# Kernel optimization log

Measured on AMD Instinct MI355X. Metric: run time of the kernel, lower is better.

The kernel has to match this reference:

```python
import jax, jax.numpy as jnp
import numpy as np
from jax import lax

B, T, F_IN = 8, 512, 229
C1 = 48            # model_size_conv // 16
C3 = 96            # model_size_conv // 8
D_CONV = 768       # model_size_conv
D_LSTM = 768       # model_size_lstm
N_PITCH = 88       # MAX_MIDI - MIN_MIDI + 1
N_STATE = 5
EMB = 2
LSTM_IN = D_CONV + N_PITCH * EMB   # 944
FC_IN = C3 * (F_IN // 4)           # 96 * 57 = 5472
BN_EPS = 1e-5


def setup_inputs() -> dict:
    key = jax.random.key(0)
    ks = iter(jax.random.split(key, 64))
    nrm = lambda shape, s=0.05: jax.random.normal(next(ks), shape, jnp.float32) * s
    uni = lambda shape: jax.random.uniform(next(ks), shape, jnp.float32, 0.5, 1.5)
    inp = {
        'mel': jax.random.normal(next(ks), (B, T, F_IN), jnp.float32),
        'conv1_w': nrm((C1, 1, 3, 3)), 'conv1_b': nrm((C1,)),
        'bn1_g': uni((C1,)), 'bn1_b': nrm((C1,)), 'bn1_m': nrm((C1,), 0.1), 'bn1_v': uni((C1,)),
        'conv2_w': nrm((C1, C1, 3, 3)), 'conv2_b': nrm((C1,)),
        'bn2_g': uni((C1,)), 'bn2_b': nrm((C1,)), 'bn2_m': nrm((C1,), 0.1), 'bn2_v': uni((C1,)),
        'conv3_w': nrm((C3, C1, 3, 3)), 'conv3_b': nrm((C3,)),
        'bn3_g': uni((C3,)), 'bn3_b': nrm((C3,)), 'bn3_m': nrm((C3,), 0.1), 'bn3_v': uni((C3,)),
        'fc_w': nrm((D_CONV, FC_IN)), 'fc_b': nrm((D_CONV,)),
        'wih1': nrm((4 * D_LSTM, LSTM_IN)), 'whh1': nrm((4 * D_LSTM, D_LSTM)),
        'bih1': nrm((4 * D_LSTM,)), 'bhh1': nrm((4 * D_LSTM,)),
        'wih2': nrm((4 * D_LSTM, D_LSTM)), 'whh2': nrm((4 * D_LSTM, D_LSTM)),
        'bih2': nrm((4 * D_LSTM,)), 'bhh2': nrm((4 * D_LSTM,)),
        'post_w': nrm((N_PITCH * N_STATE, D_LSTM)), 'post_b': nrm((N_PITCH * N_STATE,)),
        'emb_w': nrm((N_STATE, EMB), 1.0),
    }
    return inp


def _conv_bn_relu(x, w, b, g, be, m, v):
    # x: NCHW, w: OIHW, padding 'SAME' == padding=1 for 3x3
    y = lax.conv_general_dilated(x, w, (1, 1), 'SAME', dimension_numbers=('NCHW', 'OIHW', 'NCHW'))
    y = y + b[None, :, None, None]
    scale = (g / jnp.sqrt(v + BN_EPS))[None, :, None, None]
    y = (y - m[None, :, None, None]) * scale + be[None, :, None, None]
    return jax.nn.relu(y)


def _maxpool12(x):
    # MaxPool2d((1,2)) on NCHW, floor mode
    return lax.reduce_window(x, -jnp.inf, lax.max, (1, 1, 1, 2), (1, 1, 1, 2), 'VALID')


def _lstm_cell(x, h, c, wih, whh, bih, bhh):
    z = x @ wih.T + h @ whh.T + bih + bhh
    i, f, g, o = jnp.split(z, 4, axis=-1)
    c = jax.nn.sigmoid(f) * c + jax.nn.sigmoid(i) * jnp.tanh(g)
    h = jax.nn.sigmoid(o) * jnp.tanh(c)
    return h, c


def _forward(mel, conv1_w, conv1_b, bn1_g, bn1_b, bn1_m, bn1_v,
             conv2_w, conv2_b, bn2_g, bn2_b, bn2_m, bn2_v,
             conv3_w, conv3_b, bn3_g, bn3_b, bn3_m, bn3_v,
             fc_w, fc_b, wih1, whh1, bih1, bhh1, wih2, whh2, bih2, bhh2,
             post_w, post_b, emb_w):
    b = mel.shape[0]
    # --- ConvStack acoustic model (eval mode: dropout = identity) ---
    x = mel[:, None]                                  # (B,1,T,F)
    x = _conv_bn_relu(x, conv1_w, conv1_b, bn1_g, bn1_b, bn1_m, bn1_v)
    x = _conv_bn_relu(x, conv2_w, conv2_b, bn2_g, bn2_b, bn2_m, bn2_v)
    x = _maxpool12(x)
    x = _conv_bn_relu(x, conv3_w, conv3_b, bn3_g, bn3_b, bn3_m, bn3_v)
    x = _maxpool12(x)                                 # (B,C3,T,F//4)
    x = x.transpose(0, 2, 1, 3).reshape(b, -1, FC_IN) # (B,T,C3*F//4)
    acoustic = x @ fc_w.T + fc_b                      # (B,T,768)

    def step(carry, a_t):
        h1, c1, h2, c2, prev = carry                  # prev: (B,88) int32
        emb = emb_w[prev].reshape(prev.shape[0], N_PITCH * EMB)
        xt = jnp.concatenate([a_t, emb], axis=-1)     # (B,944)
        h1n, c1n = _lstm_cell(xt, h1, c1, wih1, whh1, bih1, bhh1)
        h2n, c2n = _lstm_cell(h1n, h2, c2, wih2, whh2, bih2, bhh2)
        logits = (h2n @ post_w.T + post_b).reshape(-1, N_PITCH, N_STATE)
        nprev = jnp.argmax(logits, axis=-1).astype(jnp.int32)  # argmax(softmax)==argmax(logits)
        return (h1n, c1n, h2n, c2n, nprev), logits

    z = jnp.zeros((b, D_LSTM), mel.dtype)
    prev0 = jnp.zeros((b, N_PITCH), jnp.int32)
    _, logits = lax.scan(step, (z, z, z, z, prev0), acoustic.transpose(1, 0, 2))
    return logits.transpose(1, 0, 2, 3)               # (B,T,88,N_STATE)


def reference(mel, conv1_w, conv1_b, bn1_g, bn1_b, bn1_m, bn1_v,
              conv2_w, conv2_b, bn2_g, bn2_b, bn2_m, bn2_v,
              conv3_w, conv3_b, bn3_g, bn3_b, bn3_m, bn3_v,
              fc_w, fc_b, wih1, whh1, bih1, bhh1, wih2, whh2, bih2, bhh2,
              post_w, post_b, emb_w):
    return _forward(mel, conv1_w, conv1_b, bn1_g, bn1_b, bn1_m, bn1_v,
                    conv2_w, conv2_b, bn2_g, bn2_b, bn2_m, bn2_v,
                    conv3_w, conv3_b, bn3_g, bn3_b, bn3_m, bn3_v,
                    fc_w, fc_b, wih1, whh1, bih1, bhh1, wih2, whh2, bih2, bhh2,
                    post_w, post_b, emb_w)
```

## Files before the change

kernel.cpp:

```cpp
#include <hip/hip_runtime.h>
#include <math.h>

#define WS_C3   0u
#define WS_C2CH 22413312u
#define WS_AC   28104192u
#define WS_A1   0u
#define WS_ST   31249920u

__device__ __forceinline__ float sigm(float x){ return 1.0f / (1.0f + expf(-x)); }

__device__ __forceinline__ void cstore(float* p, float v){
  union { float f; unsigned u; } c; c.f = v;
  __hip_atomic_store((unsigned*)p, c.u, __ATOMIC_RELAXED,
                     __HIP_MEMORY_SCOPE_SYSTEM);
}
__device__ __forceinline__ void cload64(const float* p, float& a, float& b){
  unsigned long long u = __hip_atomic_load((const unsigned long long*)p,
                          __ATOMIC_RELAXED, __HIP_MEMORY_SCOPE_SYSTEM);
  union { unsigned long long u; float f[2]; } c; c.u = u;
  a = c.f[0]; b = c.f[1];
}
__device__ __forceinline__ unsigned cloadu(const unsigned* p){
  return __hip_atomic_load(p, __ATOMIC_RELAXED, __HIP_MEMORY_SCOPE_SYSTEM);
}

#define SLOT 16
#define FLG  4112
__device__ __forceinline__ void gbar(unsigned* sy, unsigned bar, int wg){
  __syncthreads();
  const int tid = threadIdx.x;
  if (tid == 0)
    __hip_atomic_store(&sy[SLOT + wg*16], bar, __ATOMIC_RELAXED,
                       __HIP_MEMORY_SCOPE_SYSTEM);
  if (wg == 255){
    if (tid < 64){
      for (;;){
        unsigned m0 = cloadu(&sy[SLOT + (4*tid + 0)*16]);
        unsigned m1 = cloadu(&sy[SLOT + (4*tid + 1)*16]);
        unsigned m2 = cloadu(&sy[SLOT + (4*tid + 2)*16]);
        unsigned m3 = cloadu(&sy[SLOT + (4*tid + 3)*16]);
        unsigned a = m0 < m1 ? m0 : m1;
        unsigned b = m2 < m3 ? m2 : m3;
        unsigned mn = a < b ? a : b;
        if (__all(mn >= bar)) break;
        __builtin_amdgcn_s_sleep(1);
      }
    }
    __syncthreads();
    __hip_atomic_store(&sy[FLG + tid*16], bar, __ATOMIC_RELAXED,
                       __HIP_MEMORY_SCOPE_SYSTEM);
  } else {
    if (tid == 0){
      while (cloadu(&sy[FLG + wg*16]) < bar)
        __builtin_amdgcn_s_sleep(1);
    }
  }
  __syncthreads();
}

__global__ __launch_bounds__(256) void conv2f_k(
    const float* __restrict__ mel, const float* __restrict__ w1,
    const float* __restrict__ b1, const float* __restrict__ g1,
    const float* __restrict__ be1, const float* __restrict__ m1,
    const float* __restrict__ v1,
    const float* __restrict__ w2, const float* __restrict__ b2,
    const float* __restrict__ g2, const float* __restrict__ be2,
    const float* __restrict__ m2, const float* __restrict__ v2,
    float* __restrict__ c2ch, int t0)
{
  __shared__ float act[3*8*240];
  __shared__ float w2s[48*8*12];
  __shared__ float mel5[5*240];
  __shared__ float w1s[48*12];
  __shared__ float sc1[48], sh1[48], sc2[48], sh2[48];
  int tid = threadIdx.x;
  int b = blockIdx.x / 130, lt = blockIdx.x - b*130;
  int t = t0 - 1 + lt;

  int fg = tid % 29, ocg = tid / 29;
  int f0 = fg * 8, oc0 = ocg * 6;

  if (t < 0 || t > 511){
    if (tid < 232){
      for (int o = 0; o < 6; ++o)
        for (int jj = 0; jj < 4; ++jj){
          int fp = fg*4 + jj;
          if (fp < 114)
            c2ch[((b*48 + oc0 + o)*130 + lt)*114 + fp] = 0.f;
        }
    }
    return;
  }

  for (int idx = tid; idx < 5*240; idx += 256){
    int rr = idx / 240, w = idx - rr*240;
    int tt = t + rr - 2, f = w - 2;
    mel5[idx] = (tt >= 0 && tt < 512 && f >= 0 && f < 229)
                ? mel[(b*512 + tt)*229 + f] : 0.f;
  }
  for (int idx = tid; idx < 48*12; idx += 256){
    int c = idx / 12, q = idx - c*12;
    int kh = q >> 2, kw = q & 3;
    w1s[idx] = (kw < 3) ? w1[c*9 + kh*3 + kw] : 0.f;
  }
  if (tid < 48){
    float s1 = g1[tid] / sqrtf(v1[tid] + 1e-5f);
    sc1[tid] = s1; sh1[tid] = be1[tid] + (b1[tid] - m1[tid]) * s1;
    float s2 = g2[tid] / sqrtf(v2[tid] + 1e-5f);
    sc2[tid] = s2; sh2[tid] = be2[tid] + (b2[tid] - m2[tid]) * s2;
  }

  float acc[6][8];
  #pragma unroll
  for (int o = 0; o < 6; ++o)
    #pragma unroll
    for (int j = 0; j < 8; ++j) acc[o][j] = 0.f;

  for (int ch = 0; ch < 6; ++ch){
    int ci0 = ch * 8;
    __syncthreads();
    for (int idx = tid; idx < 3*8*240; idx += 256){
      int rr = idx / 1920;
      int rem = idx - rr*1920;
      int ci = rem / 240, w = rem - ci*240;
      int tt = t + rr - 1, f = w - 1;
      float val = 0.f;
      if (tt >= 0 && tt < 512 && f >= 0 && f < 229){
        int cg = ci0 + ci;
        float a = 0.f;
        #pragma unroll
        for (int dh = 0; dh < 3; ++dh){
          const float* mr = &mel5[(rr + dh)*240 + w];
          a = fmaf(mr[0], w1s[cg*12 + dh*4 + 0], a);
          a = fmaf(mr[1], w1s[cg*12 + dh*4 + 1], a);
          a = fmaf(mr[2], w1s[cg*12 + dh*4 + 2], a);
        }
        a = a * sc1[cg] + sh1[cg];
        val = a > 0.f ? a : 0.f;
      }
      act[idx] = val;
    }
    for (int idx = tid; idx < 48*8*12; idx += 256){
      int oc = idx / 96;
      int rem = idx - oc*96;
      int ci = rem / 12, q = rem - ci*12;
      int kh = q >> 2, kw = q & 3;
      w2s[idx] = (kw < 3) ? w2[(oc*48 + ci0 + ci)*9 + kh*3 + kw] : 0.f;
    }
    __syncthreads();
    if (tid < 232){
      for (int ci = 0; ci < 8; ++ci){
        #pragma unroll
        for (int kh = 0; kh < 3; ++kh){
          const float* ap = &act[(kh*8 + ci)*240 + f0];
          float4 A0 = *(const float4*)(ap);
          float4 A1v = *(const float4*)(ap + 4);
          float4 A2 = *(const float4*)(ap + 8);
          float L[12] = {A0.x,A0.y,A0.z,A0.w,A1v.x,A1v.y,A1v.z,A1v.w,A2.x,A2.y,A2.z,A2.w};
          #pragma unroll
          for (int o = 0; o < 6; ++o){
            float4 wv = *(const float4*)&w2s[((oc0 + o)*8 + ci)*12 + kh*4];
            #pragma unroll
            for (int j = 0; j < 8; ++j)
              acc[o][j] = fmaf(L[j+2], wv.z, fmaf(L[j+1], wv.y, fmaf(L[j], wv.x, acc[o][j])));
          }
        }
      }
    }
  }
  __syncthreads();
  if (tid < 232){
    #pragma unroll
    for (int o = 0; o < 6; ++o){
      int oc = oc0 + o;
      float s = sc2[oc], hs = sh2[oc];
      #pragma unroll
      for (int jj = 0; jj < 4; ++jj){
        int fp = fg*4 + jj;
        if (fp < 114){
          float v0 = acc[o][2*jj] * s + hs;   v0 = v0 > 0.f ? v0 : 0.f;
          float v1 = acc[o][2*jj+1] * s + hs; v1 = v1 > 0.f ? v1 : 0.f;
          c2ch[((b*48 + oc)*130 + lt)*114 + fp] = v0 > v1 ? v0 : v1;
        }
      }
    }
  }
}

__global__ __launch_bounds__(256) void conv3_k(
    const float* __restrict__ c2ch, const float* __restrict__ w3,
    const float* __restrict__ b3, const float* __restrict__ g3,
    const float* __restrict__ be3, const float* __restrict__ m3,
    const float* __restrict__ v3, float* __restrict__ c3p, int t0)
{
  __shared__ float act[3*8*128];
  __shared__ float w3s[96*8*12];
  __shared__ float sc[96], sh[96];
  int tid = threadIdx.x;
  int b = blockIdx.x >> 7, tl = blockIdx.x & 127;
  int t = t0 + tl;
  if (tid < 96){
    float s = g3[tid] / sqrtf(v3[tid] + 1e-5f);
    sc[tid] = s; sh[tid] = be3[tid] + (b3[tid] - m3[tid]) * s;
  }
  int fg = tid % 15, ocg = tid / 15;
  int f0 = fg * 8, oc0 = ocg * 6;
  float acc[6][8];
  #pragma unroll
  for (int o = 0; o < 6; ++o)
    #pragma unroll
    for (int j = 0; j < 8; ++j) acc[o][j] = 0.f;

  for (int ch = 0; ch < 6; ++ch){
    int ci0 = ch * 8;
    __syncthreads();
    for (int idx = tid; idx < 3*8*128; idx += 256){
      int rr = idx >> 10;
      int rem = idx & 1023;
      int ci = rem >> 7, w = rem & 127;
      int lt = tl + rr;
      int f = w - 1;
      float val = 0.f;
      if (f >= 0 && f < 114)
        val = c2ch[((b*48 + ci0 + ci)*130 + lt)*114 + f];
      act[idx] = val;
    }
    for (int idx = tid; idx < 96*8*12; idx += 256){
      int oc = idx / 96;
      int rem = idx - oc*96;
      int ci = rem / 12, q = rem - ci*12;
      int kh = q >> 2, kw = q & 3;
      w3s[idx] = (kw < 3) ? w3[(oc*48 + ci0 + ci)*9 + kh*3 + kw] : 0.f;
    }
    __syncthreads();
    if (tid < 240){
      for (int ci = 0; ci < 8; ++ci){
        #pragma unroll
        for (int kh = 0; kh < 3; ++kh){
          const float* ap = &act[(kh*8 + ci)*128 + f0];
          float4 A0 = *(const float4*)(ap);
          float4 A1v = *(const float4*)(ap + 4);
          float4 A2 = *(const float4*)(ap + 8);
          float L[12] = {A0.x,A0.y,A0.z,A0.w,A1v.x,A1v.y,A1v.z,A1v.w,A2.x,A2.y,A2.z,A2.w};
          #pragma unroll
          for (int o = 0; o < 6; ++o){
            float4 wv = *(const float4*)&w3s[((oc0 + o)*8 + ci)*12 + kh*4];
            #pragma unroll
            for (int j = 0; j < 8; ++j)
              acc[o][j] = fmaf(L[j+2], wv.z, fmaf(L[j+1], wv.y, fmaf(L[j], wv.x, acc[o][j])));
          }
        }
      }
    }
  }
  __syncthreads();
  if (tid < 240){
    #pragma unroll
    for (int o = 0; o < 6; ++o){
      int oc = oc0 + o;
      float s = sc[oc], hs = sh[oc];
      #pragma unroll
      for (int jj = 0; jj < 4; ++jj){
        int fp = fg*4 + jj;
        if (fp < 57){
          float v0 = acc[o][2*jj] * s + hs;   v0 = v0 > 0.f ? v0 : 0.f;
          float v1 = acc[o][2*jj+1] * s + hs; v1 = v1 > 0.f ? v1 : 0.f;
          c3p[((b*96 + oc)*512 + t)*57 + fp] = v0 > v1 ? v0 : v1;
        }
      }
    }
  }
}

__global__ __launch_bounds__(256) void gemm_fc_k(
    const float* __restrict__ c3p, const float* __restrict__ fcw,
    const float* __restrict__ fcb, float* __restrict__ ac)
{
  __shared__ float As[16*132];
  __shared__ float Bs[16*132];
  int tid = threadIdx.x;
  int m0 = blockIdx.x * 128, n0 = blockIdx.y * 128;
  int tm = (tid & 15) * 8, tn = (tid >> 4) * 8;
  float acc[8][8];
  #pragma unroll
  for (int i = 0; i < 8; ++i)
    #pragma unroll
    for (int j = 0; j < 8; ++j) acc[i][j] = 0.f;

  for (int k0 = 0; k0 < 5472; k0 += 16){
    __syncthreads();
    #pragma unroll
    for (int i = 0; i < 8; ++i){
      int idx = i*256 + tid;
      int k = idx & 15, mm = idx >> 4;
      int gk = k0 + k;
      int ci = (gk * 36793) >> 21;
      int f  = gk - ci*57;
      int gm = m0 + mm;
      int bb = gm >> 9, tt = gm & 511;
      As[k*132 + mm] = c3p[((bb*96 + ci)*512 + tt)*57 + f];
      Bs[k*132 + mm] = fcw[(n0 + mm)*5472 + gk];
    }
    __syncthreads();
    #pragma unroll
    for (int k = 0; k < 16; ++k){
      const float* arow = &As[k*132 + tm];
      const float* brow = &Bs[k*132 + tn];
      float4 a0 = *(const float4*)arow, a1 = *(const float4*)(arow + 4);
      float4 b0 = *(const float4*)brow, b1 = *(const float4*)(brow + 4);
      float av[8] = {a0.x,a0.y,a0.z,a0.w,a1.x,a1.y,a1.z,a1.w};
      float bv[8] = {b0.x,b0.y,b0.z,b0.w,b1.x,b1.y,b1.z,b1.w};
      #pragma unroll
      for (int i = 0; i < 8; ++i)
        #pragma unroll
        for (int j = 0; j < 8; ++j)
          acc[i][j] = fmaf(av[i], bv[j], acc[i][j]);
    }
  }
  #pragma unroll
  for (int i = 0; i < 8; ++i){
    int gm = m0 + tm + i;
    #pragma unroll
    for (int j = 0; j < 8; ++j){
      int gn = n0 + tn + j;
      ac[gm*768 + gn] = acc[i][j] + fcb[gn];
    }
  }
}

__global__ __launch_bounds__(256) void gemm_a1_k(
    const float* __restrict__ ac, const float* __restrict__ wih1,
    const float* __restrict__ bih1, const float* __restrict__ bhh1,
    float* __restrict__ A1)
{
  __shared__ float As[16*132];
  __shared__ float Bs[16*132];
  int tid = threadIdx.x;
  int m0 = blockIdx.x * 128, n0 = blockIdx.y * 128;
  int tm = (tid & 15) * 8, tn = (tid >> 4) * 8;
  float acc[8][8];
  #pragma unroll
  for (int i = 0; i < 8; ++i)
    #pragma unroll
    for (int j = 0; j < 8; ++j) acc[i][j] = 0.f;

  for (int k0 = 0; k0 < 768; k0 += 16){
    __syncthreads();
    #pragma unroll
    for (int i = 0; i < 8; ++i){
      int idx = i*256 + tid;
      int k = idx & 15, mm = idx >> 4;
      int gk = k0 + k;
      As[k*132 + mm] = ac[(m0 + mm)*768 + gk];
      Bs[k*132 + mm] = wih1[(n0 + mm)*944 + gk];
    }
    __syncthreads();
    #pragma unroll
    for (int k = 0; k < 16; ++k){
      const float* arow = &As[k*132 + tm];
      const float* brow = &Bs[k*132 + tn];
      float4 a0 = *(const float4*)arow, a1 = *(const float4*)(arow + 4);
      float4 b0 = *(const float4*)brow, b1 = *(const float4*)(brow + 4);
      float av[8] = {a0.x,a0.y,a0.z,a0.w,a1.x,a1.y,a1.z,a1.w};
      float bv[8] = {b0.x,b0.y,b0.z,b0.w,b1.x,b1.y,b1.z,b1.w};
      #pragma unroll
      for (int i = 0; i < 8; ++i)
        #pragma unroll
        for (int j = 0; j < 8; ++j)
          acc[i][j] = fmaf(av[i], bv[j], acc[i][j]);
    }
  }
  #pragma unroll
  for (int i = 0; i < 8; ++i){
    int gm = m0 + tm + i;
    int tt = gm & 511, bb = gm >> 9;
    #pragma unroll
    for (int j = 0; j < 8; ++j){
      int gn = n0 + tn + j;
      A1[tt*24576 + gn*8 + bb] = acc[i][j] + bih1[gn] + bhh1[gn];
    }
  }
}

#define SA 948
#define S2 772
__global__ __launch_bounds__(256, 1) void rec_k(
    const float* __restrict__ A1,
    const float* __restrict__ whh1, const float* __restrict__ wih1,
    const float* __restrict__ wih2, const float* __restrict__ whh2,
    const float* __restrict__ bih2, const float* __restrict__ bhh2,
    const float* __restrict__ postw, const float* __restrict__ postb,
    const float* __restrict__ embw,
    float* __restrict__ xbuf, float* __restrict__ h2b,
    unsigned* __restrict__ sy, float* __restrict__ out)
{
  const int wg = blockIdx.x, tid = threadIdx.x;
  const int wv = tid >> 6, l = tid & 63;
  __shared__ float xs[8*SA];
  __shared__ float h2s[8*S2];
  __shared__ float zbuf[96];
  __shared__ float red2[160];

  float wA[15][3];
  float wB[24][3];
  float wC[3][5];
  {
    int Rb = wv*768 + wg*3;
    #pragma unroll
    for (int ki = 0; ki < 15; ++ki){
      int k = l + (ki << 6);
      #pragma unroll
      for (int u = 0; u < 3; ++u){
        float w = 0.f;
        if (k < 768) w = whh1[(Rb + u)*768 + k];
        else if (k < 944) w = wih1[(Rb + u)*944 + k];
        wA[ki][u] = w;
      }
    }
    #pragma unroll
    for (int ki = 0; ki < 24; ++ki){
      int k = l + (ki << 6);
      #pragma unroll
      for (int u = 0; u < 3; ++u)
        wB[ki][u] = (k < 768) ? wih2[(Rb + u)*768 + k] : whh2[(Rb + u)*768 + k - 768];
    }
  }
  if (wg < 88){
    #pragma unroll
    for (int kc = 0; kc < 3; ++kc)
      #pragma unroll
      for (int s = 0; s < 5; ++s)
        wC[kc][s] = postw[(wg*5 + s)*768 + tid + (kc << 8)];
  }
  float b2r = 0.f; int fR = 0, fb = 0;
  if (tid < 96){
    int g = tid / 24, rem = tid - g*24;
    int u = rem >> 3; fb = rem & 7;
    fR = g*768 + wg*3 + u;
    b2r = bih2[fR] + bhh2[fR];
  }
  float pbr = (wg < 88 && tid < 40) ? postb[wg*5 + (tid >> 3)] : 0.f;
  float c1r = 0.f, c2r = 0.f;

  for (int idx = tid; idx < 8*S2; idx += 256) h2s[idx] = 0.f;
  if (wg == 0){
    for (int idx = tid; idx < 1408; idx += 256){
      int e = idx >> 3, bb = idx & 7;
      cstore(&xbuf[(768 + e)*8 + bb], embw[e & 1]);
    }
  }
  unsigned bar = 1;
  gbar(sy, bar, wg);

  for (int t = 0; t < 512; ++t){
    const int cur = t & 1, nxt = cur ^ 1;
    float* xc  = xbuf + cur * 7552;
    float* xn  = xbuf + nxt * 7552;
    float* h2n = h2b + nxt * 6144;

    float a1v = 0.f;
    if (tid < 96) a1v = A1[t*24576 + fR*8 + fb];

    {
      for (int idx = tid; idx < 3776; idx += 256){
        float a, b; cload64(xc + 2*idx, a, b);
        int k = idx >> 2, p = (idx & 3) << 1;
        xs[p*SA + k]       = a;
        xs[(p + 1)*SA + k] = b;
      }
      __syncthreads();
      float acc[3][8];
      #pragma unroll
      for (int u = 0; u < 3; ++u)
        #pragma unroll
        for (int j = 0; j < 8; ++j) acc[u][j] = 0.f;
      #pragma unroll
      for (int ki = 0; ki < 15; ++ki){
        int k = l + (ki << 6);
        if (k < 944){
          float x0 = xs[k],        x1 = xs[SA + k],   x2 = xs[2*SA + k], x3 = xs[3*SA + k];
          float x4 = xs[4*SA + k], x5 = xs[5*SA + k], x6 = xs[6*SA + k], x7 = xs[7*SA + k];
          #pragma unroll
          for (int u = 0; u < 3; ++u){
            float w = wA[ki][u];
            acc[u][0] = fmaf(w, x0, acc[u][0]);
            acc[u][1] = fmaf(w, x1, acc[u][1]);
            acc[u][2] = fmaf(w, x2, acc[u][2]);
            acc[u][3] = fmaf(w, x3, acc[u][3]);
            acc[u][4] = fmaf(w, x4, acc[u][4]);
            acc[u][5] = fmaf(w, x5, acc[u][5]);
            acc[u][6] = fmaf(w, x6, acc[u][6]);
            acc[u][7] = fmaf(w, x7, acc[u][7]);
          }
        }
      }
      #pragma unroll
      for (int u = 0; u < 3; ++u)
        #pragma unroll
        for (int j = 0; j < 8; ++j){
          float s = acc[u][j];
          s += __shfl_xor(s, 1);  s += __shfl_xor(s, 2);  s += __shfl_xor(s, 4);
          s += __shfl_xor(s, 8);  s += __shfl_xor(s, 16); s += __shfl_xor(s, 32);
          if (l == 0) zbuf[wv*24 + u*8 + j] = s;
        }
      __syncthreads();
      if (tid < 96)
        zbuf[tid] += a1v;
      __syncthreads();
      if (tid < 24){
        float zi = zbuf[tid], zf = zbuf[24 + tid], zg = zbuf[48 + tid], zo = zbuf[72 + tid];
        c1r = sigm(zf)*c1r + sigm(zi)*tanhf(zg);
        float hh = sigm(zo)*tanhf(c1r);
        cstore(&xn[(wg*3 + (tid >> 3))*8 + (tid & 7)], hh);
      }
      ++bar; gbar(sy, bar, wg);
    }

    {
      for (int idx = tid; idx < 3072; idx += 256){
        float a, b; cload64(xn + 2*idx, a, b);
        int k = idx >> 2, p = (idx & 3) << 1;
        xs[p*S2 + k]       = a;
        xs[(p + 1)*S2 + k] = b;
      }
      __syncthreads();
      float acc[3][8];
      #pragma unroll
      for (int u = 0; u < 3; ++u)
        #pragma unroll
        for (int j = 0; j < 8; ++j) acc[u][j] = 0.f;
      #pragma unroll
      for (int ki = 0; ki < 24; ++ki){
        float x0, x1, x2, x3, x4, x5, x6, x7;
        if (ki < 12){
          int k = l + (ki << 6);
          x0 = xs[k];        x1 = xs[S2 + k];   x2 = xs[2*S2 + k]; x3 = xs[3*S2 + k];
          x4 = xs[4*S2 + k]; x5 = xs[5*S2 + k]; x6 = xs[6*S2 + k]; x7 = xs[7*S2 + k];
        } else {
          int k = l + ((ki - 12) << 6);
          x0 = h2s[k];        x1 = h2s[S2 + k];   x2 = h2s[2*S2 + k]; x3 = h2s[3*S2 + k];
          x4 = h2s[4*S2 + k]; x5 = h2s[5*S2 + k]; x6 = h2s[6*S2 + k]; x7 = h2s[7*S2 + k];
        }
        #pragma unroll
        for (int u = 0; u < 3; ++u){
          float w = wB[ki][u];
          acc[u][0] = fmaf(w, x0, acc[u][0]);
          acc[u][1] = fmaf(w, x1, acc[u][1]);
          acc[u][2] = fmaf(w, x2, acc[u][2]);
          acc[u][3] = fmaf(w, x3, acc[u][3]);
          acc[u][4] = fmaf(w, x4, acc[u][4]);
          acc[u][5] = fmaf(w, x5, acc[u][5]);
          acc[u][6] = fmaf(w, x6, acc[u][6]);
          acc[u][7] = fmaf(w, x7, acc[u][7]);
        }
      }
      #pragma unroll
      for (int u = 0; u < 3; ++u)
        #pragma unroll
        for (int j = 0; j < 8; ++j){
          float s = acc[u][j];
          s += __shfl_xor(s, 1);  s += __shfl_xor(s, 2);  s += __shfl_xor(s, 4);
          s += __shfl_xor(s, 8);  s += __shfl_xor(s, 16); s += __shfl_xor(s, 32);
          if (l == 0) zbuf[wv*24 + u*8 + j] = s;
        }
      __syncthreads();
      if (tid < 96)
        zbuf[tid] += b2r;
      __syncthreads();
      if (tid < 24){
        float zi = zbuf[tid], zf = zbuf[24 + tid], zg = zbuf[48 + tid], zo = zbuf[72 + tid];
        c2r = sigm(zf)*c2r + sigm(zi)*tanhf(zg);
        float hh = sigm(zo)*tanhf(c2r);
        cstore(&h2n[(wg*3 + (tid >> 3))*8 + (tid & 7)], hh);
      }
      ++bar; gbar(sy, bar, wg);
    }

    {
      for (int idx = tid; idx < 3072; idx += 256){
        float a, b; cload64(h2n + 2*idx, a, b);
        int k = idx >> 2, p = (idx & 3) << 1;
        h2s[p*S2 + k]       = a;
        h2s[(p + 1)*S2 + k] = b;
      }
      __syncthreads();
      if (wg < 88){
        float acc[5][8];
        #pragma unroll
        for (int s = 0; s < 5; ++s)
          #pragma unroll
          for (int j = 0; j < 8; ++j) acc[s][j] = 0.f;
        #pragma unroll
        for (int kc = 0; kc < 3; ++kc){
          int k = tid + (kc << 8);
          float x0 = h2s[k],        x1 = h2s[S2 + k],   x2 = h2s[2*S2 + k], x3 = h2s[3*S2 + k];
          float x4 = h2s[4*S2 + k], x5 = h2s[5*S2 + k], x6 = h2s[6*S2 + k], x7 = h2s[7*S2 + k];
          #pragma unroll
          for (int s = 0; s < 5; ++s){
            float w = wC[kc][s];
            acc[s][0] = fmaf(w, x0, acc[s][0]);
            acc[s][1] = fmaf(w, x1, acc[s][1]);
            acc[s][2] = fmaf(w, x2, acc[s][2]);
            acc[s][3] = fmaf(w, x3, acc[s][3]);
            acc[s][4] = fmaf(w, x4, acc[s][4]);
            acc[s][5] = fmaf(w, x5, acc[s][5]);
            acc[s][6] = fmaf(w, x6, acc[s][6]);
            acc[s][7] = fmaf(w, x7, acc[s][7]);
          }
        }
        #pragma unroll
        for (int s = 0; s < 5; ++s)
          #pragma unroll
          for (int j = 0; j < 8; ++j){
            float v = acc[s][j];
            v += __shfl_xor(v, 1);  v += __shfl_xor(v, 2);  v += __shfl_xor(v, 4);
            v += __shfl_xor(v, 8);  v += __shfl_xor(v, 16); v += __shfl_xor(v, 32);
            if (l == 0) red2[(s*8 + j)*4 + wv] = v;
          }
        __syncthreads();
        if (tid < 40){
          float sum = red2[tid*4] + red2[tid*4 + 1] + red2[tid*4 + 2] + red2[tid*4 + 3] + pbr;
          int s = tid >> 3, bb = tid & 7;
          out[bb*225280 + t*440 + wg*5 + s] = sum;
          zbuf[tid] = sum;
        }
        __syncthreads();
        if (tid < 8){
          float best = zbuf[tid]; int bs = 0;
          #pragma unroll
          for (int s = 1; s < 5; ++s){
            float v = zbuf[s*8 + tid];
            if (v > best){ best = v; bs = s; }
          }
          cstore(&xn[(768 + wg*2)*8 + tid],     embw[bs*2]);
          cstore(&xn[(768 + wg*2 + 1)*8 + tid], embw[bs*2 + 1]);
        }
      }
      ++bar; gbar(sy, bar, wg);
    }
  }
}

extern "C" void kernel_launch(void* const* d_in, const int* in_sizes, int n_in,
                              void* d_out, int out_size, void* d_ws, size_t ws_size,
                              hipStream_t stream)
{
  (void)in_sizes; (void)n_in; (void)out_size; (void)ws_size;
  const float* mel  = (const float*)d_in[0];
  const float* w1   = (const float*)d_in[1];
  const float* b1   = (const float*)d_in[2];
  const float* g1   = (const float*)d_in[3];
  const float* be1  = (const float*)d_in[4];
  const float* m1   = (const float*)d_in[5];
  const float* v1   = (const float*)d_in[6];
  const float* w2   = (const float*)d_in[7];
  const float* b2   = (const float*)d_in[8];
  const float* g2   = (const float*)d_in[9];
  const float* be2  = (const float*)d_in[10];
  const float* m2   = (const float*)d_in[11];
  const float* v2   = (const float*)d_in[12];
  const float* w3   = (const float*)d_in[13];
  const float* b3   = (const float*)d_in[14];
  const float* g3   = (const float*)d_in[15];
  const float* be3  = (const float*)d_in[16];
  const float* m3   = (const float*)d_in[17];
  const float* v3   = (const float*)d_in[18];
  const float* fcw  = (const float*)d_in[19];
  const float* fcb  = (const float*)d_in[20];
  const float* wih1 = (const float*)d_in[21];
  const float* whh1 = (const float*)d_in[22];
  const float* bih1 = (const float*)d_in[23];
  const float* bhh1 = (const float*)d_in[24];
  const float* wih2 = (const float*)d_in[25];
  const float* whh2 = (const float*)d_in[26];
  const float* bih2 = (const float*)d_in[27];
  const float* bhh2 = (const float*)d_in[28];
  const float* postw= (const float*)d_in[29];
  const float* postb= (const float*)d_in[30];
  const float* embw = (const float*)d_in[31];

  float* ws    = (float*)d_ws;
  float* c3p   = ws + WS_C3;
  float* c2ch  = ws + WS_C2CH;
  float* ac    = ws + WS_AC;
  float* A1    = ws + WS_A1;
  float* st    = ws + WS_ST;
  float* xbuf  = st;
  float* h2b   = st + 15104;
  unsigned* sy = (unsigned*)(st + 27392);
  float* outp  = (float*)d_out;

  hipMemsetAsync(st, 0, 35600 * sizeof(float), stream);

  for (int c = 0; c < 4; ++c){
    int t0 = c * 128;
    conv2f_k<<<dim3(8*130), dim3(256), 0, stream>>>(
        mel, w1, b1, g1, be1, m1, v1, w2, b2, g2, be2, m2, v2, c2ch, t0);
    conv3_k<<<dim3(8*128), dim3(256), 0, stream>>>(
        c2ch, w3, b3, g3, be3, m3, v3, c3p, t0);
  }
  gemm_fc_k<<<dim3(32, 6), dim3(256), 0, stream>>>(c3p, fcw, fcb, ac);
  gemm_a1_k<<<dim3(32, 24), dim3(256), 0, stream>>>(ac, wih1, bih1, bhh1, A1);

  rec_k<<<dim3(256), dim3(256), 0, stream>>>(
      A1, whh1, wih1, wih2, whh2, bih2, bhh2, postw, postb, embw,
      xbuf, h2b, sy, outp);
}
```

Measured before the change: 22.30 ms.

## Halve recurrent grid to 128 wider blocks with decentralized grid barrier

The persistent LSTM kernel now runs 128 blocks of 512 threads, each owning 6 hidden units instead of 3, and the gate-row mapping and reductions are adjusted to match. The grid barrier drops the master-block gather/broadcast: every block polls all 128 arrival slots directly, removing one hop per barrier. Layer-1 input staging reuses the h1 values already loaded into shared memory during the previous step's layer-2 phase, so only the embedding part is reloaded. Keeping the weights in registers at 512 threads per block with launch bounds (512,2) tightens the register budget, which risks spills, and all blocks now poll the sync slots at once.

```diff
diff --git a/kernel.cpp b/kernel.cpp
--- a/kernel.cpp
+++ b/kernel.cpp
@@ -24,35 +24,19 @@
   return __hip_atomic_load(p, __ATOMIC_RELAXED, __HIP_MEMORY_SCOPE_SYSTEM);
 }
 
-#define SLOT 16
-#define FLG  4112
 __device__ __forceinline__ void gbar(unsigned* sy, unsigned bar, int wg){
   __syncthreads();
   const int tid = threadIdx.x;
   if (tid == 0)
-    __hip_atomic_store(&sy[SLOT + wg*16], bar, __ATOMIC_RELAXED,
+    __hip_atomic_store(&sy[16 + wg*16], bar, __ATOMIC_RELAXED,
                        __HIP_MEMORY_SCOPE_SYSTEM);
-  if (wg == 255){
-    if (tid < 64){
-      for (;;){
-        unsigned m0 = cloadu(&sy[SLOT + (4*tid + 0)*16]);
-        unsigned m1 = cloadu(&sy[SLOT + (4*tid + 1)*16]);
-        unsigned m2 = cloadu(&sy[SLOT + (4*tid + 2)*16]);
-        unsigned m3 = cloadu(&sy[SLOT + (4*tid + 3)*16]);
-        unsigned a = m0 < m1 ? m0 : m1;
-        unsigned b = m2 < m3 ? m2 : m3;
-        unsigned mn = a < b ? a : b;
-        if (__all(mn >= bar)) break;
-        __builtin_amdgcn_s_sleep(1);
-      }
-    }
-    __syncthreads();
-    __hip_atomic_store(&sy[FLG + tid*16], bar, __ATOMIC_RELAXED,
-                       __HIP_MEMORY_SCOPE_SYSTEM);
-  } else {
-    if (tid == 0){
-      while (cloadu(&sy[FLG + wg*16]) < bar)
-        __builtin_amdgcn_s_sleep(1);
+  if (tid < 64){
+    for (;;){
+      unsigned m0 = cloadu(&sy[16 + (2*tid)*16]);
+      unsigned m1 = cloadu(&sy[16 + (2*tid + 1)*16]);
+      unsigned mn = m0 < m1 ? m0 : m1;
+      if (__all(mn >= bar)) break;
+      __builtin_amdgcn_s_sleep(1);
     }
   }
   __syncthreads();
@@ -382,9 +366,9 @@
   }
 }
 
-#define SA 948
-#define S2 772
-__global__ __launch_bounds__(256, 1) void rec_k(
+#define S 948
+#define SH 772
+__global__ __launch_bounds__(512, 2) void rec_k(
     const float* __restrict__ A1,
     const float* __restrict__ whh1, const float* __restrict__ wih1,
     const float* __restrict__ wih2, const float* __restrict__ whh2,
@@ -396,55 +380,58 @@
 {
   const int wg = blockIdx.x, tid = threadIdx.x;
   const int wv = tid >> 6, l = tid & 63;
-  __shared__ float xs[8*SA];
-  __shared__ float h2s[8*S2];
-  __shared__ float zbuf[96];
-  __shared__ float red2[160];
-
+  __shared__ float xs[8*S];
+  __shared__ float h2s[8*SH];
+  __shared__ float zbuf[192];
+  __shared__ float red2[320];
+
+  int grow[3];
+  #pragma unroll
+  for (int u = 0; u < 3; ++u){
+    int r = 3*wv + u;
+    grow[u] = (r/6)*768 + wg*6 + (r%6);
+  }
   float wA[15][3];
+  #pragma unroll
+  for (int ki = 0; ki < 15; ++ki){
+    int k = l + (ki << 6);
+    #pragma unroll
+    for (int u = 0; u < 3; ++u){
+      float w = 0.f;
+      if (k < 768) w = whh1[grow[u]*768 + k];
+      else if (k < 944) w = wih1[grow[u]*944 + k];
+      wA[ki][u] = w;
+    }
+  }
   float wB[24][3];
-  float wC[3][5];
-  {
-    int Rb = wv*768 + wg*3;
-    #pragma unroll
-    for (int ki = 0; ki < 15; ++ki){
-      int k = l + (ki << 6);
-      #pragma unroll
-      for (int u = 0; u < 3; ++u){
-        float w = 0.f;
-        if (k < 768) w = whh1[(Rb + u)*768 + k];
-        else if (k < 944) w = wih1[(Rb + u)*944 + k];
-        wA[ki][u] = w;
-      }
-    }
-    #pragma unroll
-    for (int ki = 0; ki < 24; ++ki){
-      int k = l + (ki << 6);
-      #pragma unroll
-      for (int u = 0; u < 3; ++u)
-        wB[ki][u] = (k < 768) ? wih2[(Rb + u)*768 + k] : whh2[(Rb + u)*768 + k - 768];
-    }
-  }
+  #pragma unroll
+  for (int ki = 0; ki < 24; ++ki){
+    int k = l + (ki << 6);
+    #pragma unroll
+    for (int u = 0; u < 3; ++u)
+      wB[ki][u] = (k < 768) ? wih2[grow[u]*768 + k] : whh2[grow[u]*768 + k - 768];
+  }
+  float wCa[5], wCb[5];
   if (wg < 88){
     #pragma unroll
-    for (int kc = 0; kc < 3; ++kc)
-      #pragma unroll
-      for (int s = 0; s < 5; ++s)
-        wC[kc][s] = postw[(wg*5 + s)*768 + tid + (kc << 8)];
+    for (int s = 0; s < 5; ++s){
+      wCa[s] = postw[(wg*5 + s)*768 + tid];
+      wCb[s] = (tid < 256) ? postw[(wg*5 + s)*768 + 512 + tid] : 0.f;
+    }
   }
   float b2r = 0.f; int fR = 0, fb = 0;
-  if (tid < 96){
-    int g = tid / 24, rem = tid - g*24;
-    int u = rem >> 3; fb = rem & 7;
-    fR = g*768 + wg*3 + u;
+  if (tid < 192){
+    int r = tid >> 3; fb = tid & 7;
+    fR = (r/6)*768 + wg*6 + (r%6);
     b2r = bih2[fR] + bhh2[fR];
   }
   float pbr = (wg < 88 && tid < 40) ? postb[wg*5 + (tid >> 3)] : 0.f;
   float c1r = 0.f, c2r = 0.f;
 
-  for (int idx = tid; idx < 8*S2; idx += 256) h2s[idx] = 0.f;
+  for (int idx = tid; idx < 8*S; idx += 512) xs[idx] = 0.f;
+  for (int idx = tid; idx < 8*SH; idx += 512) h2s[idx] = 0.f;
   if (wg == 0){
-    for (int idx = tid; idx < 1408; idx += 256){
+    for (int idx = tid; idx < 1408; idx += 512){
       int e = idx >> 3, bb = idx & 7;
       cstore(&xbuf[(768 + e)*8 + bb], embw[e & 1]);
     }
@@ -459,14 +446,19 @@
     float* h2n = h2b + nxt * 6144;
 
     float a1v = 0.f;
-    if (tid < 96) a1v = A1[t*24576 + fR*8 + fb];
+    if (tid < 192) a1v = A1[t*24576 + fR*8 + fb];
 
     {
-      for (int idx = tid; idx < 3776; idx += 256){
-        float a, b; cload64(xc + 2*idx, a, b);
-        int k = idx >> 2, p = (idx & 3) << 1;
-        xs[p*SA + k]       = a;
-        xs[(p + 1)*SA + k] = b;
+      #pragma unroll
+      for (int it = 0; it < 2; ++it){
+        int idx = tid + it*512;
+        if (idx < 704){
+          int idx64 = 3072 + idx;
+          float a, b; cload64(xc + 2*idx64, a, b);
+          int k = idx64 >> 2, p = (idx64 & 3) << 1;
+          xs[p*S + k]       = a;
+          xs[(p + 1)*S + k] = b;
+        }
       }
       __syncthreads();
       float acc[3][8];
@@ -478,8 +470,8 @@
       for (int ki = 0; ki < 15; ++ki){
         int k = l + (ki << 6);
         if (k < 944){
-          float x0 = xs[k],        x1 = xs[SA + k],   x2 = xs[2*SA + k], x3 = xs[3*SA + k];
-          float x4 = xs[4*SA + k], x5 = xs[5*SA + k], x6 = xs[6*SA + k], x7 = xs[7*SA + k];
+          float x0 = xs[k],       x1 = xs[S + k],   x2 = xs[2*S + k], x3 = xs[3*S + k];
+          float x4 = xs[4*S + k], x5 = xs[5*S + k], x6 = xs[6*S + k], x7 = xs[7*S + k];
           #pragma unroll
           for (int u = 0; u < 3; ++u){
             float w = wA[ki][u];
@@ -501,27 +493,31 @@
           float s = acc[u][j];
           s += __shfl_xor(s, 1);  s += __shfl_xor(s, 2);  s += __shfl_xor(s, 4);
           s += __shfl_xor(s, 8);  s += __shfl_xor(s, 16); s += __shfl_xor(s, 32);
-          if (l == 0) zbuf[wv*24 + u*8 + j] = s;
+          if (l == 0) zbuf[(3*wv + u)*8 + j] = s;
         }
       __syncthreads();
-      if (tid < 96)
+      if (tid < 192)
         zbuf[tid] += a1v;
       __syncthreads();
-      if (tid < 24){
-        float zi = zbuf[tid], zf = zbuf[24 + tid], zg = zbuf[48 + tid], zo = zbuf[72 + tid];
+      if (tid < 48){
+        int u = tid >> 3, b = tid & 7;
+        float zi = zbuf[u*8 + b],        zf = zbuf[(6 + u)*8 + b];
+        float zg = zbuf[(12 + u)*8 + b], zo = zbuf[(18 + u)*8 + b];
         c1r = sigm(zf)*c1r + sigm(zi)*tanhf(zg);
         float hh = sigm(zo)*tanhf(c1r);
-        cstore(&xn[(wg*3 + (tid >> 3))*8 + (tid & 7)], hh);
+        cstore(&xn[(wg*6 + u)*8 + b], hh);
       }
       ++bar; gbar(sy, bar, wg);
     }
 
     {
-      for (int idx = tid; idx < 3072; idx += 256){
-        float a, b; cload64(xn + 2*idx, a, b);
-        int k = idx >> 2, p = (idx & 3) << 1;
-        xs[p*S2 + k]       = a;
-        xs[(p + 1)*S2 + k] = b;
+      #pragma unroll
+      for (int it = 0; it < 6; ++it){
+        int idx64 = tid + it*512;
+        float a, b; cload64(xn + 2*idx64, a, b);
+        int k = idx64 >> 2, p = (idx64 & 3) << 1;
+        xs[p*S + k]       = a;
+        xs[(p + 1)*S + k] = b;
       }
       __syncthreads();
       float acc[3][8];
@@ -534,12 +530,12 @@
         float x0, x1, x2, x3, x4, x5, x6, x7;
         if (ki < 12){
           int k = l + (ki << 6);
-          x0 = xs[k];        x1 = xs[S2 + k];   x2 = xs[2*S2 + k]; x3 = xs[3*S2 + k];
-          x4 = xs[4*S2 + k]; x5 = xs[5*S2 + k]; x6 = xs[6*S2 + k]; x7 = xs[7*S2 + k];
+          x0 = xs[k];       x1 = xs[S + k];   x2 = xs[2*S + k]; x3 = xs[3*S + k];
+          x4 = xs[4*S + k]; x5 = xs[5*S + k]; x6 = xs[6*S + k]; x7 = xs[7*S + k];
         } else {
           int k = l + ((ki - 12) << 6);
-          x0 = h2s[k];        x1 = h2s[S2 + k];   x2 = h2s[2*S2 + k]; x3 = h2s[3*S2 + k];
-          x4 = h2s[4*S2 + k]; x5 = h2s[5*S2 + k]; x6 = h2s[6*S2 + k]; x7 = h2s[7*S2 + k];
+          x0 = h2s[k];        x1 = h2s[SH + k];   x2 = h2s[2*SH + k]; x3 = h2s[3*SH + k];
+          x4 = h2s[4*SH + k]; x5 = h2s[5*SH + k]; x6 = h2s[6*SH + k]; x7 = h2s[7*SH + k];
         }
         #pragma unroll
         for (int u = 0; u < 3; ++u){
@@ -561,27 +557,31 @@
           float s = acc[u][j];
           s += __shfl_xor(s, 1);  s += __shfl_xor(s, 2);  s += __shfl_xor(s, 4);
           s += __shfl_xor(s, 8);  s += __shfl_xor(s, 16); s += __shfl_xor(s, 32);
-          if (l == 0) zbuf[wv*24 + u*8 + j] = s;
+          if (l == 0) zbuf[(3*wv + u)*8 + j] = s;
         }
       __syncthreads();
-      if (tid < 96)
+      if (tid < 192)
         zbuf[tid] += b2r;
       __syncthreads();
-      if (tid < 24){
-        float zi = zbuf[tid], zf = zbuf[24 + tid], zg = zbuf[48 + tid], zo = zbuf[72 + tid];
+      if (tid < 48){
+        int u = tid >> 3, b = tid & 7;
+        float zi = zbuf[u*8 + b],        zf = zbuf[(6 + u)*8 + b];
+        float zg = zbuf[(12 + u)*8 + b], zo = zbuf[(18 + u)*8 + b];
         c2r = sigm(zf)*c2r + sigm(zi)*tanhf(zg);
         float hh = sigm(zo)*tanhf(c2r);
-        cstore(&h2n[(wg*3 + (tid >> 3))*8 + (tid & 7)], hh);
+        cstore(&h2n[(wg*6 + u)*8 + b], hh);
       }
       ++bar; gbar(sy, bar, wg);
     }
 
     {
-      for (int idx = tid; idx < 3072; idx += 256){
-        float a, b; cload64(h2n + 2*idx, a, b);
-        int k = idx >> 2, p = (idx & 3) << 1;
-        h2s[p*S2 + k]       = a;
-        h2s[(p + 1)*S2 + k] = b;
+      #pragma unroll
+      for (int it = 0; it < 6; ++it){
+        int idx64 = tid + it*512;
+        float a, b; cload64(h2n + 2*idx64, a, b);
+        int k = idx64 >> 2, p = (idx64 & 3) << 1;
+        h2s[p*SH + k]       = a;
+        h2s[(p + 1)*SH + k] = b;
       }
       __syncthreads();
       if (wg < 88){
@@ -590,14 +590,13 @@
         for (int s = 0; s < 5; ++s)
           #pragma unroll
           for (int j = 0; j < 8; ++j) acc[s][j] = 0.f;
-        #pragma unroll
-        for (int kc = 0; kc < 3; ++kc){
-          int k = tid + (kc << 8);
-          float x0 = h2s[k],        x1 = h2s[S2 + k],   x2 = h2s[2*S2 + k], x3 = h2s[3*S2 + k];
-          float x4 = h2s[4*S2 + k], x5 = h2s[5*S2 + k], x6 = h2s[6*S2 + k], x7 = h2s[7*S2 + k];
+        {
+          int k = tid;
+          float x0 = h2s[k],        x1 = h2s[SH + k],   x2 = h2s[2*SH + k], x3 = h2s[3*SH + k];
+          float x4 = h2s[4*SH + k], x5 = h2s[5*SH + k], x6 = h2s[6*SH + k], x7 = h2s[7*SH + k];
           #pragma unroll
           for (int s = 0; s < 5; ++s){
-            float w = wC[kc][s];
+            float w = wCa[s];
             acc[s][0] = fmaf(w, x0, acc[s][0]);
             acc[s][1] = fmaf(w, x1, acc[s][1]);
             acc[s][2] = fmaf(w, x2, acc[s][2]);
@@ -608,6 +607,23 @@
             acc[s][7] = fmaf(w, x7, acc[s][7]);
           }
         }
+        if (tid < 256){
+          int k = tid + 512;
+          float x0 = h2s[k],        x1 = h2s[SH + k],   x2 = h2s[2*SH + k], x3 = h2s[3*SH + k];
+          float x4 = h2s[4*SH + k], x5 = h2s[5*SH + k], x6 = h2s[6*SH + k], x7 = h2s[7*SH + k];
+          #pragma unroll
+          for (int s = 0; s < 5; ++s){
+            float w = wCb[s];
+            acc[s][0] = fmaf(w, x0, acc[s][0]);
+            acc[s][1] = fmaf(w, x1, acc[s][1]);
+            acc[s][2] = fmaf(w, x2, acc[s][2]);
+            acc[s][3] = fmaf(w, x3, acc[s][3]);
+            acc[s][4] = fmaf(w, x4, acc[s][4]);
+            acc[s][5] = fmaf(w, x5, acc[s][5]);
+            acc[s][6] = fmaf(w, x6, acc[s][6]);
+            acc[s][7] = fmaf(w, x7, acc[s][7]);
+          }
+        }
         #pragma unroll
         for (int s = 0; s < 5; ++s)
           #pragma unroll
@@ -615,11 +631,13 @@
             float v = acc[s][j];
             v += __shfl_xor(v, 1);  v += __shfl_xor(v, 2);  v += __shfl_xor(v, 4);
             v += __shfl_xor(v, 8);  v += __shfl_xor(v, 16); v += __shfl_xor(v, 32);
-            if (l == 0) red2[(s*8 + j)*4 + wv] = v;
+            if (l == 0) red2[(s*8 + j)*8 + wv] = v;
           }
         __syncthreads();
         if (tid < 40){
-          float sum = red2[tid*4] + red2[tid*4 + 1] + red2[tid*4 + 2] + red2[tid*4 + 3] + pbr;
+          float sum = pbr;
+          #pragma unroll
+          for (int q = 0; q < 8; ++q) sum += red2[tid*8 + q];
           int s = tid >> 3, bb = tid & 7;
           out[bb*225280 + t*440 + wg*5 + s] = sum;
           zbuf[tid] = sum;
@@ -690,7 +708,7 @@
   unsigned* sy = (unsigned*)(st + 27392);
   float* outp  = (float*)d_out;
 
-  hipMemsetAsync(st, 0, 35600 * sizeof(float), stream);
+  hipMemsetAsync(st, 0, 29696 * sizeof(float), stream);
 
   for (int c = 0; c < 4; ++c){
     int t0 = c * 128;
@@ -702,7 +720,7 @@
   gemm_fc_k<<<dim3(32, 6), dim3(256), 0, stream>>>(c3p, fcw, fcb, ac);
   gemm_a1_k<<<dim3(32, 24), dim3(256), 0, stream>>>(ac, wih1, bih1, bhh1, A1);
 
-  rec_k<<<dim3(256), dim3(256), 0, stream>>>(
+  rec_k<<<dim3(128), dim3(512), 0, stream>>>(
       A1, whh1, wih1, wih2, whh2, bih2, bhh2, postw, postb, embw,
       xbuf, h2b, sy, outp);
 }
```

Measured after the change: 34.52 ms. 54.8% more time.
